# Kernel optimization log

Measured on AMD Instinct MI355X. Metric: run time of the kernel, lower is better.

## Reference

```python
import jax, jax.numpy as jnp
import numpy as np

NUM_HEADS = 1
MAX_LEVELS = 2
NUM_POINTS = 4


def _grid_sample_zeros(img, gx, gy):
    """Bilinear grid sample, align_corners=False, zero padding.
    img: [C,H,W]; gx, gy: [Q,P] normalized coords in [-1,1]. Returns [C,Q,P]."""
    C, H, W = img.shape
    ix = (gx + 1.0) * (W * 0.5) - 0.5
    iy = (gy + 1.0) * (H * 0.5) - 0.5
    x0 = jnp.floor(ix)
    y0 = jnp.floor(iy)
    x1 = x0 + 1.0
    y1 = y0 + 1.0

    def gather(yi, xi):
        valid = (xi >= 0) & (xi < W) & (yi >= 0) & (yi < H)
        xc = jnp.clip(xi, 0, W - 1).astype(jnp.int32)
        yc = jnp.clip(yi, 0, H - 1).astype(jnp.int32)
        return img[:, yc, xc] * valid[None].astype(img.dtype)  # [C,Q,P]

    w00 = ((x1 - ix) * (y1 - iy))[None]
    w01 = ((ix - x0) * (y1 - iy))[None]
    w10 = ((x1 - ix) * (iy - y0))[None]
    w11 = ((ix - x0) * (iy - y0))[None]
    return (gather(y0, x0) * w00 + gather(y0, x1) * w01 +
            gather(y1, x0) * w10 + gather(y1, x1) * w11)


def setup_inputs() -> dict:
    key = jax.random.key(0)
    ks = jax.random.split(key, 8)
    C, Q, Lv, H_, W_ = 256, 40000, 2, 128, 256
    Nv = H_ * W_
    query = jax.random.normal(ks[0], (1, Q, C), dtype=jnp.float32)
    k_unused = jax.random.normal(ks[1], (Lv, Nv, C), dtype=jnp.float32)
    value = jax.random.normal(ks[2], (Lv, Nv, C), dtype=jnp.float32)
    reference_points = jax.random.uniform(ks[3], (1, Q, Lv, 2), dtype=jnp.float32)
    spatial_shapes = jnp.array([[H_, W_], [H_, W_]], dtype=jnp.int64)
    out_off = MAX_LEVELS * NUM_HEADS * NUM_POINTS * 2
    out_aw = MAX_LEVELS * NUM_HEADS * NUM_POINTS
    W_off = jax.random.normal(ks[4], (C, out_off), dtype=jnp.float32) * 0.02
    b_off = jnp.zeros((out_off,), dtype=jnp.float32)
    W_attn = jax.random.normal(ks[5], (C, out_aw), dtype=jnp.float32) * 0.02
    b_attn = jnp.zeros((out_aw,), dtype=jnp.float32)
    return {"query": query, "key": k_unused, "value": value,
            "reference_points": reference_points, "spatial_shapes": spatial_shapes,
            "W_off": W_off, "b_off": b_off, "W_attn": W_attn, "b_attn": b_attn}


def reference(query, key, value, reference_points, spatial_shapes, W_off, b_off, W_attn, b_attn):
    shapes = np.asarray(jax.device_get(spatial_shapes))  # static level metadata
    Lv, Nv, C = value.shape
    bs, Q, _ = query.shape  # bs == 1 (asserted by original module)

    # offsets: (bs,Q,H,L,P,2), sliced to actual number of levels
    off = (query @ W_off + b_off).reshape(bs, Q, NUM_HEADS, MAX_LEVELS, NUM_POINTS, 2)
    off = off[:, :, :, :Lv]
    # attention weights with softmax over (levels*points)
    aw = (query @ W_attn + b_attn).reshape(bs, Q, NUM_HEADS, MAX_LEVELS, NUM_POINTS)
    aw = aw[:, :, :, :Lv].reshape(bs, Q, NUM_HEADS, Lv * NUM_POINTS)
    aw = jax.nn.softmax(aw, axis=-1).reshape(bs, Q, NUM_HEADS, Lv, NUM_POINTS)

    # normalizer is (W, H) per level
    normalizer = jnp.stack([spatial_shapes[:, 1], spatial_shapes[:, 0]], -1).astype(query.dtype)
    loc = reference_points[:, :, None, :, None, :] + off / normalizer[None, None, None, :, None, :]
    grids = 2.0 * loc - 1.0  # (bs,Q,1,Lv,P,2)

    acc = jnp.zeros((Q, C), dtype=query.dtype)
    for l in range(Lv):
        H_, W_ = int(shapes[l, 0]), int(shapes[l, 1])
        img = value[l].T.reshape(C, H_, W_)
        gx = grids[0, :, 0, l, :, 0]  # [Q,P]
        gy = grids[0, :, 0, l, :, 1]
        sampled = _grid_sample_zeros(img, gx, gy)  # [C,Q,P]
        acc = acc + jnp.einsum('cqp,qp->qc', sampled, aw[0, :, 0, l])
    return acc[None]  # (1, Q, C)
```

## Files before the change

### kernel.cpp

```cpp
#include <hip/hip_runtime.h>


#define C_DIM 256
#define Q_DIM 40000
#define H_IMG 128
#define W_IMG 256
#define NV    (H_IMG * W_IMG)

#define WS_SAMPLES_OFF 0
#define WS_WT_OFF      5120000
#define WS_BIAS_OFF    5144576

__global__ __launch_bounds__(256) void setup_w_kernel(
    const float* __restrict__ Woff,  const float* __restrict__ boff,
    const float* __restrict__ Wattn, const float* __restrict__ battn,
    float* __restrict__ Wt, float* __restrict__ bias)
{
    const int tid = threadIdx.x;
    for (int i = tid; i < 4096; i += 256) {
        int c = i >> 4, j = i & 15;
        Wt[j * 256 + c] = Woff[i];
    }
    for (int i = tid; i < 2048; i += 256) {
        int c = i >> 3, j = i & 7;
        Wt[(16 + j) * 256 + c] = Wattn[i];
    }
    if (tid < 16)      bias[tid] = boff[tid];
    else if (tid < 24) bias[tid] = battn[tid - 16];
}

__global__ __launch_bounds__(256) void proj_gemm_kernel(
    const float* __restrict__ query,
    const float* __restrict__ rp,
    const float* __restrict__ Wt,
    const float* __restrict__ bias,
    float4* __restrict__ samples)
{
    __shared__ float Qt[32 * 65];
    __shared__ float Lt[64 * 25];

    const int tid = threadIdx.x;
    const int r   = tid & 63;
    const int c4  = tid >> 6;
    const int q0  = blockIdx.x * 64;

    const float* brow = bias + c4 * 6;
    float acc0 = brow[0], acc1 = brow[1], acc2 = brow[2];
    float acc3 = brow[3], acc4 = brow[4], acc5 = brow[5];

    const float* wrow = Wt + (c4 * 6) * 256;

    for (int kc = 0; kc < 8; ++kc) {
        {
            const int rw = tid >> 3;
            const int f  = tid & 7;
#pragma unroll
            for (int p = 0; p < 2; ++p) {
                const int row = rw + 32 * p;
                float4 v = *reinterpret_cast<const float4*>(
                    query + (size_t)(q0 + row) * C_DIM + kc * 32 + f * 4);
                Qt[(f * 4 + 0) * 65 + row] = v.x;
                Qt[(f * 4 + 1) * 65 + row] = v.y;
                Qt[(f * 4 + 2) * 65 + row] = v.z;
                Qt[(f * 4 + 3) * 65 + row] = v.w;
            }
        }
        __syncthreads();
        const float* wk = wrow + kc * 32;
#pragma unroll
        for (int k = 0; k < 32; ++k) {
            const float qv = Qt[k * 65 + r];
            acc0 = fmaf(wk[0 * 256 + k], qv, acc0);
            acc1 = fmaf(wk[1 * 256 + k], qv, acc1);
            acc2 = fmaf(wk[2 * 256 + k], qv, acc2);
            acc3 = fmaf(wk[3 * 256 + k], qv, acc3);
            acc4 = fmaf(wk[4 * 256 + k], qv, acc4);
            acc5 = fmaf(wk[5 * 256 + k], qv, acc5);
        }
        __syncthreads();
    }

    {
        float* Lr = Lt + r * 25 + c4 * 6;
        Lr[0] = acc0; Lr[1] = acc1; Lr[2] = acc2;
        Lr[3] = acc3; Lr[4] = acc4; Lr[5] = acc5;
    }
    __syncthreads();

    if (tid < 64) {
        const int q = q0 + tid;
        float s[24];
#pragma unroll
        for (int j = 0; j < 24; ++j) s[j] = Lt[tid * 25 + j];

        float4 rp4 = *reinterpret_cast<const float4*>(rp + (size_t)q * 4);

        float mx = s[16];
#pragma unroll
        for (int k = 1; k < 8; ++k) mx = fmaxf(mx, s[16 + k]);
        float e[8], den = 0.f;
#pragma unroll
        for (int k = 0; k < 8; ++k) { e[k] = __expf(s[16 + k] - mx); den += e[k]; }
        const float rd = 1.0f / den;

#pragma unroll
        for (int smp = 0; smp < 8; ++smp) {
            const float refx = (smp >= 4) ? rp4.z : rp4.x;
            const float refy = (smp >= 4) ? rp4.w : rp4.y;
            const float ix = refx * (float)W_IMG + s[2 * smp]     - 0.5f;
            const float iy = refy * (float)H_IMG + s[2 * smp + 1] - 0.5f;
            samples[(size_t)q * 8 + smp] = make_float4(ix, iy, e[smp] * rd, 0.f);
        }
    }
}

__global__ __launch_bounds__(256) void deform_sample_kernel(
    const float* __restrict__ value,
    const float4* __restrict__ samples,
    float* __restrict__ out)
{
    const int lane = threadIdx.x & 63;
    const int q = (blockIdx.x * blockDim.x + threadIdx.x) >> 6;
    if (q >= Q_DIM) return;

    float4 acc = make_float4(0.f, 0.f, 0.f, 0.f);

#pragma unroll
    for (int smp = 0; smp < 8; ++smp) {
        float4 rec = samples[(size_t)q * 8 + smp];
        const float* base = value + (size_t)(smp >> 2) * ((size_t)NV * C_DIM);

        float ix = rec.x, iy = rec.y, aw = rec.z;
        float x0f = floorf(ix), y0f = floorf(iy);
        float fx = ix - x0f, fy = iy - y0f;
        int x0 = (int)x0f, y0 = (int)y0f;
        int x1 = x0 + 1,   y1 = y0 + 1;

        bool vx0 = (unsigned)x0 < W_IMG;
        bool vx1 = (unsigned)x1 < W_IMG;
        bool vy0 = (unsigned)y0 < H_IMG;
        bool vy1 = (unsigned)y1 < H_IMG;

        int xc0 = min(max(x0, 0), W_IMG - 1);
        int xc1 = min(max(x1, 0), W_IMG - 1);
        int yc0 = min(max(y0, 0), H_IMG - 1);
        int yc1 = min(max(y1, 0), H_IMG - 1);

        float wx0 = 1.f - fx, wx1 = fx;
        float wy0 = 1.f - fy, wy1 = fy;
        float w00 = (vx0 && vy0) ? wx0 * wy0 * aw : 0.f;
        float w01 = (vx1 && vy0) ? wx1 * wy0 * aw : 0.f;
        float w10 = (vx0 && vy1) ? wx0 * wy1 * aw : 0.f;
        float w11 = (vx1 && vy1) ? wx1 * wy1 * aw : 0.f;

        const int ch = lane * 4;
        float4 v00 = *reinterpret_cast<const float4*>(base + (size_t)(yc0 * W_IMG + xc0) * C_DIM + ch);
        float4 v01 = *reinterpret_cast<const float4*>(base + (size_t)(yc0 * W_IMG + xc1) * C_DIM + ch);
        float4 v10 = *reinterpret_cast<const float4*>(base + (size_t)(yc1 * W_IMG + xc0) * C_DIM + ch);
        float4 v11 = *reinterpret_cast<const float4*>(base + (size_t)(yc1 * W_IMG + xc1) * C_DIM + ch);

        acc.x += w00 * v00.x + w01 * v01.x + w10 * v10.x + w11 * v11.x;
        acc.y += w00 * v00.y + w01 * v01.y + w10 * v10.y + w11 * v11.y;
        acc.z += w00 * v00.z + w01 * v01.z + w10 * v10.z + w11 * v11.z;
        acc.w += w00 * v00.w + w01 * v01.w + w10 * v10.w + w11 * v11.w;
    }

    *reinterpret_cast<float4*>(out + (size_t)q * C_DIM + lane * 4) = acc;
}

extern "C" void kernel_launch(void* const* d_in, const int* in_sizes, int n_in,
                              void* d_out, int out_size, void* d_ws, size_t ws_size,
                              hipStream_t stream) {
    const float* query = (const float*)d_in[0];
    const float* value = (const float*)d_in[2];
    const float* rp    = (const float*)d_in[3];
    const float* Woff  = (const float*)d_in[5];
    const float* boff  = (const float*)d_in[6];
    const float* Wattn = (const float*)d_in[7];
    const float* battn = (const float*)d_in[8];
    float* out = (float*)d_out;

    char* ws = (char*)d_ws;
    float4* samples = (float4*)(ws + WS_SAMPLES_OFF);
    float*  Wt      = (float*) (ws + WS_WT_OFF);
    float*  bias    = (float*) (ws + WS_BIAS_OFF);

    setup_w_kernel<<<1, 256, 0, stream>>>(Woff, boff, Wattn, battn, Wt, bias);
    proj_gemm_kernel<<<625, 256, 0, stream>>>(query, rp, Wt, bias, samples);
    const int blocks = (Q_DIM * 64 + 255) / 256;
    deform_sample_kernel<<<blocks, 256, 0, stream>>>(value, samples, out);
}
```

Baseline: 296.5 us.

## Split projection GEMM over K across waves and halve sampling launches

The projection kernel now splits the K dimension across the four waves. Each wave computes all 24 outputs for its 32-wide K slice, with the weights addressed through a wave-uniform index, and the partial sums are reduced through shared memory. This is meant to cut redundant LDS reads of the query tile and let the weight loads become scalar. The sampling kernel is also launched twice, once per half of the queries, which adds launch overhead with no obvious benefit on the same stream. The larger per-thread accumulator array raises register and LDS usage.

```diff
diff --git a/kernel.cpp b/kernel.cpp
--- a/kernel.cpp
+++ b/kernel.cpp
@@ -29,69 +29,73 @@
     else if (tid < 24) bias[tid] = battn[tid - 16];
 }
 
-__global__ __launch_bounds__(256) void proj_gemm_kernel(
+__global__ __launch_bounds__(256) void proj_gemm4_kernel(
     const float* __restrict__ query,
     const float* __restrict__ rp,
     const float* __restrict__ Wt,
     const float* __restrict__ bias,
     float4* __restrict__ samples)
 {
-    __shared__ float Qt[32 * 65];
-    __shared__ float Lt[64 * 25];
+    __shared__ float Qt[128 * 65];
+    __shared__ float red[3 * 64 * 25];
 
     const int tid = threadIdx.x;
     const int r   = tid & 63;
-    const int c4  = tid >> 6;
+    const int wv  = tid >> 6;
+    const int wu  = __builtin_amdgcn_readfirstlane(wv);
     const int q0  = blockIdx.x * 64;
 
-    const float* brow = bias + c4 * 6;
-    float acc0 = brow[0], acc1 = brow[1], acc2 = brow[2];
-    float acc3 = brow[3], acc4 = brow[4], acc5 = brow[5];
-
-    const float* wrow = Wt + (c4 * 6) * 256;
-
-    for (int kc = 0; kc < 8; ++kc) {
+    float acc[24];
+#pragma unroll
+    for (int j = 0; j < 24; ++j) acc[j] = 0.f;
+
+#pragma unroll
+    for (int p = 0; p < 2; ++p) {
         {
-            const int rw = tid >> 3;
-            const int f  = tid & 7;
-#pragma unroll
-            for (int p = 0; p < 2; ++p) {
-                const int row = rw + 32 * p;
-                float4 v = *reinterpret_cast<const float4*>(
-                    query + (size_t)(q0 + row) * C_DIM + kc * 32 + f * 4);
-                Qt[(f * 4 + 0) * 65 + row] = v.x;
-                Qt[(f * 4 + 1) * 65 + row] = v.y;
-                Qt[(f * 4 + 2) * 65 + row] = v.z;
-                Qt[(f * 4 + 3) * 65 + row] = v.w;
+            const int row = tid >> 2;
+            const int k0  = (tid & 3) * 32;
+            const float* src = query + (size_t)(q0 + row) * C_DIM + p * 128 + k0;
+#pragma unroll
+            for (int iq = 0; iq < 8; ++iq) {
+                float4 v = *reinterpret_cast<const float4*>(src + iq * 4);
+                Qt[(k0 + iq * 4 + 0) * 65 + row] = v.x;
+                Qt[(k0 + iq * 4 + 1) * 65 + row] = v.y;
+                Qt[(k0 + iq * 4 + 2) * 65 + row] = v.z;
+                Qt[(k0 + iq * 4 + 3) * 65 + row] = v.w;
             }
         }
         __syncthreads();
-        const float* wk = wrow + kc * 32;
-#pragma unroll
-        for (int k = 0; k < 32; ++k) {
-            const float qv = Qt[k * 65 + r];
-            acc0 = fmaf(wk[0 * 256 + k], qv, acc0);
-            acc1 = fmaf(wk[1 * 256 + k], qv, acc1);
-            acc2 = fmaf(wk[2 * 256 + k], qv, acc2);
-            acc3 = fmaf(wk[3 * 256 + k], qv, acc3);
-            acc4 = fmaf(wk[4 * 256 + k], qv, acc4);
-            acc5 = fmaf(wk[5 * 256 + k], qv, acc5);
+
+        const int kk0 = wu * 32;
+        const int kg0 = p * 128 + wu * 32;
+#pragma unroll
+        for (int i = 0; i < 32; ++i) {
+            const float qv = Qt[(kk0 + i) * 65 + r];
+#pragma unroll
+            for (int j = 0; j < 24; ++j) {
+                acc[j] = fmaf(Wt[j * 256 + kg0 + i], qv, acc[j]);
+            }
         }
         __syncthreads();
     }
 
-    {
-        float* Lr = Lt + r * 25 + c4 * 6;
-        Lr[0] = acc0; Lr[1] = acc1; Lr[2] = acc2;
-        Lr[3] = acc3; Lr[4] = acc4; Lr[5] = acc5;
+    if (wv > 0) {
+        float* dst = red + ((wv - 1) * 64 + r) * 25;
+#pragma unroll
+        for (int j = 0; j < 24; ++j) dst[j] = acc[j];
     }
     __syncthreads();
 
     if (tid < 64) {
-        const int q = q0 + tid;
+        const int q = q0 + r;
         float s[24];
 #pragma unroll
-        for (int j = 0; j < 24; ++j) s[j] = Lt[tid * 25 + j];
+        for (int j = 0; j < 24; ++j) {
+            s[j] = acc[j] + bias[j]
+                 + red[(0 * 64 + r) * 25 + j]
+                 + red[(1 * 64 + r) * 25 + j]
+                 + red[(2 * 64 + r) * 25 + j];
+        }
 
         float4 rp4 = *reinterpret_cast<const float4*>(rp + (size_t)q * 4);
 
@@ -117,11 +121,13 @@
 __global__ __launch_bounds__(256) void deform_sample_kernel(
     const float* __restrict__ value,
     const float4* __restrict__ samples,
-    float* __restrict__ out)
+    float* __restrict__ out,
+    int q_base, int q_count)
 {
     const int lane = threadIdx.x & 63;
-    const int q = (blockIdx.x * blockDim.x + threadIdx.x) >> 6;
-    if (q >= Q_DIM) return;
+    const int qi = (blockIdx.x * blockDim.x + threadIdx.x) >> 6;
+    if (qi >= q_count) return;
+    const int q = q_base + qi;
 
     float4 acc = make_float4(0.f, 0.f, 0.f, 0.f);
 
@@ -186,7 +192,10 @@
     float*  bias    = (float*) (ws + WS_BIAS_OFF);
 
     setup_w_kernel<<<1, 256, 0, stream>>>(Woff, boff, Wattn, battn, Wt, bias);
-    proj_gemm_kernel<<<625, 256, 0, stream>>>(query, rp, Wt, bias, samples);
-    const int blocks = (Q_DIM * 64 + 255) / 256;
-    deform_sample_kernel<<<blocks, 256, 0, stream>>>(value, samples, out);
-}
+    proj_gemm4_kernel<<<625, 256, 0, stream>>>(query, rp, Wt, bias, samples);
+
+    const int qh = Q_DIM / 2;
+    const int blocks_h = (qh * 64 + 255) / 256;
+    deform_sample_kernel<<<blocks_h, 256, 0, stream>>>(value, samples, out, 0,  qh);
+    deform_sample_kernel<<<blocks_h, 256, 0, stream>>>(value, samples, out, qh, qh);
+}
```

New measurement: 275.6 us. 1.08x faster.
